# Kernel optimization log

Measured on AMD Instinct MI355X. Metric: run time of the kernel, lower is better.

The kernel has to match this reference:

```python
import jax, jax.numpy as jnp
import numpy as np

N = 100000
E = 1600000
IN_DIM = 128
HID = 128
OUT_DIM = 64
ORDER = 4


def setup_inputs() -> dict:
    key = jax.random.key(0)
    ks = jax.random.split(key, 10)
    x = jax.random.normal(ks[0], (N, IN_DIM), dtype=jnp.float32)
    edge_index = jax.random.randint(ks[1], (2, E), 0, N, dtype=jnp.int64)
    gen_edge_index = jax.random.randint(ks[2], (2, E), 0, N, dtype=jnp.int64)
    s = 1.0 / np.sqrt(IN_DIM)
    w_orig = jax.random.normal(ks[3], (ORDER + 1, IN_DIM, HID), dtype=jnp.float32) * s
    b_orig = jax.random.normal(ks[4], (ORDER + 1, HID), dtype=jnp.float32) * s
    w_aug = jax.random.normal(ks[5], (ORDER + 1, IN_DIM, HID), dtype=jnp.float32) * s
    b_aug = jax.random.normal(ks[6], (ORDER + 1, HID), dtype=jnp.float32) * s
    fusion_weight = jnp.ones((2,), dtype=jnp.float32)
    clf_w = jax.random.normal(ks[7], (HID, OUT_DIM), dtype=jnp.float32) / np.sqrt(HID)
    clf_b = jax.random.normal(ks[8], (OUT_DIM,), dtype=jnp.float32) / np.sqrt(HID)
    return {"x": x, "edge_index": edge_index, "gen_edge_index": gen_edge_index,
            "w_orig": w_orig, "b_orig": b_orig, "w_aug": w_aug, "b_aug": b_aug,
            "fusion_weight": fusion_weight, "clf_w": clf_w, "clf_b": clf_b}


def _beta_wavelet(x, edge_index, W, b, num_nodes):
    # add self loops
    loop = jnp.arange(num_nodes, dtype=edge_index.dtype)
    row = jnp.concatenate([edge_index[0], loop])
    col = jnp.concatenate([edge_index[1], loop])
    # symmetric normalization D^{-1/2} A D^{-1/2}
    deg = jax.ops.segment_sum(jnp.ones_like(col, dtype=x.dtype), col, num_segments=num_nodes)
    dinv = jnp.where(deg > 0, deg ** -0.5, 0.0)
    norm = dinv[row] * dinv[col]  # [E+N]
    out = x @ W[0] + b[0]
    Tx = x
    for i in range(1, ORDER + 1):
        msg = norm[:, None] * Tx[row]                      # gather + scale [E+N, D]
        Tx = jax.ops.segment_sum(msg, col, num_segments=num_nodes)  # scatter_add
        out = out + Tx @ W[i] + b[i]
    return jax.nn.relu(out)


def reference(x, edge_index, gen_edge_index, w_orig, b_orig, w_aug, b_aug, fusion_weight, clf_w, clf_b):
    num_nodes = x.shape[0]
    h_orig = _beta_wavelet(x, edge_index, w_orig, b_orig, num_nodes)
    h_aug = _beta_wavelet(x, gen_edge_index, w_aug, b_aug, num_nodes)
    w = jax.nn.softmax(fusion_weight)
    h_final = w[0] * h_orig + w[1] * h_aug
    return h_final @ clf_w + clf_b
```

## Files before the change

kernel.cpp:

```cpp
#include <hip/hip_runtime.h>

#define N_NODES 100000
#define NPAD    100096
#define NE      1600000
#define DIM     128
#define ODIM    64
#define NORDER  4
#define KTOT    640
#define NB      391

typedef _Float16 h8 __attribute__((ext_vector_type(8)));
typedef float f4 __attribute__((ext_vector_type(4)));

__device__ __forceinline__ float2 up2(unsigned p) {
    union { unsigned u; _Float16 h[2]; } c; c.u = p;
    return make_float2((float)c.h[0], (float)c.h[1]);
}
__device__ __forceinline__ unsigned pk2(float x, float y) {
    union { unsigned u; _Float16 h[2]; } c;
    c.h[0] = (_Float16)x; c.h[1] = (_Float16)y;
    return c.u;
}
__device__ __forceinline__ unsigned short f2hbits(float x) {
    union { _Float16 h; unsigned short s; } c;
    c.h = (_Float16)x;
    return c.s;
}
__device__ __forceinline__ void async_cp16(const void* g, void* l) {
    __builtin_amdgcn_global_load_lds((const __attribute__((address_space(1))) void*)g,
                                     (__attribute__((address_space(3))) void*)l, 16, 0, 0);
}


__global__ __launch_bounds__(256) void hist_edges(const int* __restrict__ e0,
                                                  const int* __restrict__ e1,
                                                  int* __restrict__ bhist) {
    __shared__ int lh[NB];
    int t = threadIdx.x;
    int g = blockIdx.x >= 782;
    int blk = g ? (blockIdx.x - 782) : blockIdx.x;
    const int* colp = (g ? e1 : e0) + NE;
    int* bh = bhist + g * NB;
    for (int i = t; i < NB; i += 256) lh[i] = 0;
    __syncthreads();
    int base = blk * 2048 + t;
#pragma unroll
    for (int j = 0; j < 8; ++j) {
        int e = base + j * 256;
        if (e < NE) atomicAdd(&lh[colp[e] >> 8], 1);
    }
    __syncthreads();
    for (int i = t; i < NB; i += 256) if (lh[i]) atomicAdd(&bh[i], lh[i]);
}

__global__ void wave_scan(const int* __restrict__ in,
                          int* __restrict__ oexcl,
                          int* __restrict__ ocur,
                          int n, int with_cur) {
    int wv = threadIdx.x >> 6, lane = threadIdx.x & 63;
    if (wv >= 2) return;
    const int* I = in + wv * n;
    int* O = oexcl + wv * (n + 1);
    int* C = ocur + wv * n;
    int carry = 0;
    for (int base = 0; base < n; base += 64) {
        int i = base + lane;
        int v = (i < n) ? I[i] : 0;
        int s = v;
#pragma unroll
        for (int off = 1; off < 64; off <<= 1) {
            int x = __shfl_up(s, off, 64);
            if (lane >= off) s += x;
        }
        int excl = carry + s - v;
        if (i < n) {
            O[i] = excl;
            if (with_cur) C[i] = excl;
        }
        carry += __shfl(s, 63, 64);
    }
    if (lane == 0) O[n] = carry;
}

__global__ __launch_bounds__(256) void part_edges(const int* __restrict__ e0,
                                                  const int* __restrict__ e1,
                                                  int* __restrict__ bcursor,
                                                  unsigned* __restrict__ pairs) {
    __shared__ int lh[NB];
    __shared__ int lpos[NB];
    int t = threadIdx.x;
    int g = blockIdx.x >= NB;
    int blk = g ? (blockIdx.x - NB) : blockIdx.x;
    const int* rowp = (g ? e1 : e0);
    const int* colp = rowp + NE;
    int* bc = bcursor + g * NB;
    unsigned* pr = pairs + (size_t)g * NE;
    for (int i = t; i < NB; i += 256) lh[i] = 0;
    __syncthreads();
    int base = blk * 4096 + t;
    int rank[16];
    short bk[16];
    unsigned char lcv[16];
#pragma unroll
    for (int j = 0; j < 16; ++j) {
        int e = base + j * 256;
        rank[j] = -1;
        if (e < NE) {
            int c = colp[e];
            bk[j] = (short)(c >> 8);
            lcv[j] = (unsigned char)(c & 255);
            rank[j] = atomicAdd(&lh[c >> 8], 1);
        }
    }
    __syncthreads();
    for (int i = t; i < NB; i += 256) {
        int n = lh[i];
        lpos[i] = n ? atomicAdd(&bc[i], n) : 0;
    }
    __syncthreads();
#pragma unroll
    for (int j = 0; j < 16; ++j) {
        int e = base + j * 256;
        if (e < NE) {
            int b = bk[j];
            pr[lpos[b] + rank[j]] = ((unsigned)rowp[e] << 8) | lcv[j];
        }
    }
}

__global__ __launch_bounds__(256) void cnt_scan(const unsigned* __restrict__ pairs,
                                                const int* __restrict__ boff,
                                                int* __restrict__ ptrv,
                                                float* __restrict__ dinv,
                                                int* __restrict__ bsum) {
    __shared__ int lcnt[256];
    __shared__ int lscan[256];
    int t = threadIdx.x;
    int g = blockIdx.x >= NB;
    int b = g ? (blockIdx.x - NB) : blockIdx.x;
    const unsigned* pr = pairs + (size_t)g * NE;
    const int* bo = boff + g * (NB + 1);
    int* pv = ptrv + g * (N_NODES + 1);
    float* dv = dinv + g * N_NODES;
    int* bs = bsum + g * NB;
    lcnt[t] = 0;
    __syncthreads();
    int s = bo[b], e = bo[b + 1];
    for (int i = s + t; i < e; i += 256)
        atomicAdd(&lcnt[pr[i] & 255u], 1);
    __syncthreads();
    int v = lcnt[t];
    lscan[t] = v;
    __syncthreads();
    for (int off = 1; off < 256; off <<= 1) {
        int x = (t >= off) ? lscan[t - off] : 0;
        __syncthreads();
        lscan[t] += x;
        __syncthreads();
    }
    int node = (b << 8) + t;
    if (node < N_NODES) {
        pv[node] = lscan[t] - v;
        dv[node] = rsqrtf((float)(v + 1));
    }
    if (t == 255) bs[b] = lscan[255];
}

__global__ __launch_bounds__(256) void scan_addk(int* __restrict__ ptrv,
                                                 const int* __restrict__ bmid) {
    int t = threadIdx.x;
    int g = blockIdx.x >= NB;
    int b = g ? (blockIdx.x - NB) : blockIdx.x;
    int* pv = ptrv + g * (N_NODES + 1);
    const int* bm = bmid + g * (NB + 1);
    int node = (b << 8) + t;
    if (node < N_NODES) pv[node] += bm[b];
    if (b == 0 && t == 0) pv[N_NODES] = NE;
}

__global__ __launch_bounds__(256) void fine_csr(const unsigned* __restrict__ pairs,
                                                const int* __restrict__ boff,
                                                const int* __restrict__ ptrv,
                                                int* __restrict__ srcv) {
    __shared__ int lcnt[256];
    int t = threadIdx.x;
    int g = blockIdx.x >= NB;
    int b = g ? (blockIdx.x - NB) : blockIdx.x;
    const unsigned* pr = pairs + (size_t)g * NE;
    const int* bo = boff + g * (NB + 1);
    const int* pv = ptrv + g * (N_NODES + 1);
    int* sv = srcv + (size_t)g * NE;
    lcnt[t] = 0;
    __syncthreads();
    int s = bo[b], e = bo[b + 1];
    int base = b << 8;
    for (int i = s + t; i < e; i += 256) {
        unsigned pk = pr[i];
        int lc = (int)(pk & 255u);
        int pos = pv[base + lc] + atomicAdd(&lcnt[lc], 1);
        sv[pos] = (int)(pk >> 8);
    }
}

__global__ __launch_bounds__(256) void xcast(const float* __restrict__ x,
                                             unsigned* __restrict__ Tbig) {
    int idx = blockIdx.x * 256 + threadIdx.x;
    if (idx >= NPAD * 64) return;
    int m = idx >> 6, u = idx & 63;
    int e = (m << 7) + u * 2;
    float a = (m < N_NODES) ? x[e]     : 0.f;
    float b = (m < N_NODES) ? x[e + 1] : 0.f;
    Tbig[m * 320 + u] = pk2(a, b);
}

__global__ __launch_bounds__(256) void wcast(const float* __restrict__ Wo,
                                             const float* __restrict__ Wa,
                                             unsigned short* __restrict__ Wt) {
    int idx = blockIdx.x * 256 + threadIdx.x;
    if (idx >= 2 * 5 * DIM * DIM) return;
    int g   = idx / (5 * DIM * DIM);
    int rem = idx % (5 * DIM * DIM);
    int i   = rem / (DIM * DIM);
    int r2  = rem % (DIM * DIM);
    int k8  = r2 >> 10;
    int n   = (r2 >> 3) & 127;
    int k7  = r2 & 7;
    int k   = k8 * 8 + k7;
    const float* W = g ? Wa : Wo;
    Wt[idx] = f2hbits(W[(i * DIM + k) * DIM + n]);
}

__global__ __launch_bounds__(256) void propagate(const unsigned* __restrict__ Tin,
                                                 unsigned* __restrict__ Tout,
                                                 const int* __restrict__ ptrv,
                                                 const int* __restrict__ srcv,
                                                 const float* __restrict__ dinv) {
    int gid  = blockIdx.x * 256 + threadIdx.x;
    int lane = threadIdx.x & 63;
    int v    = __builtin_amdgcn_readfirstlane(gid >> 6);
    if (v >= N_NODES) return;
    float dv = dinv[v];
    float2 self = up2(Tin[v * 320 + lane]);
    float ax = dv * dv * self.x;
    float ay = dv * dv * self.y;
    int beg = ptrv[v], end = ptrv[v + 1];
    int k = beg;
    for (; k + 16 <= end; k += 16) {
        int u[16];
#pragma unroll
        for (int j = 0; j < 16; ++j) u[j] = srcv[k + j];
        float2 tt[16];
#pragma unroll
        for (int j = 0; j < 16; ++j) tt[j] = up2(Tin[u[j] * 320 + lane]);
        float w[16];
#pragma unroll
        for (int j = 0; j < 16; ++j) w[j] = dinv[u[j]] * dv;
#pragma unroll
        for (int j = 0; j < 16; ++j) { ax += w[j] * tt[j].x; ay += w[j] * tt[j].y; }
    }
    for (; k + 4 <= end; k += 4) {
        int u[4];
#pragma unroll
        for (int j = 0; j < 4; ++j) u[j] = srcv[k + j];
        float2 tt[4];
#pragma unroll
        for (int j = 0; j < 4; ++j) tt[j] = up2(Tin[u[j] * 320 + lane]);
        float w[4];
#pragma unroll
        for (int j = 0; j < 4; ++j) w[j] = dinv[u[j]] * dv;
#pragma unroll
        for (int j = 0; j < 4; ++j) { ax += w[j] * tt[j].x; ay += w[j] * tt[j].y; }
    }
    for (; k < end; ++k) {
        int u = srcv[k];
        float w = dinv[u] * dv;
        float2 t = up2(Tin[u * 320 + lane]);
        ax += w * t.x; ay += w * t.y;
    }
    Tout[v * 320 + lane] = pk2(ax, ay);
}

__global__ __launch_bounds__(256, 3) void gemmK(const unsigned short* __restrict__ A,
                                                const unsigned short* __restrict__ Wt,
                                                float* __restrict__ C) {
    __shared__ unsigned short Bl[DIM * DIM];
    int t = threadIdx.x;
    int lane = t & 63, wv = t >> 6;
    int m0 = blockIdx.x * 128 + wv * 32;
    int l15 = lane & 15, q = lane >> 4;
    f4 acc[2][8];
#pragma unroll
    for (int mt = 0; mt < 2; ++mt)
#pragma unroll
        for (int nt = 0; nt < 8; ++nt) acc[mt][nt] = (f4)(0.f);

#pragma unroll
    for (int i = 0; i < 5; ++i) {
        const unsigned short* WtI = Wt + (size_t)i * DIM * DIM;
        h8 af[2][4];
#pragma unroll
        for (int mt = 0; mt < 2; ++mt)
#pragma unroll
            for (int kc = 0; kc < 4; ++kc)
                af[mt][kc] = *(const h8*)(A + (size_t)(m0 + mt * 16 + l15) * KTOT
                                            + i * DIM + (kc * 4 + q) * 8);
#pragma unroll
        for (int c = 0; c < 8; ++c) {
            int ci = c * 4 + wv;
            async_cp16(WtI + ci * 512 + lane * 8, &Bl[ci * 512]);
        }
        __syncthreads();
#pragma unroll
        for (int kc = 0; kc < 4; ++kc) {
            int c = kc * 4 + q;
#pragma unroll
            for (int nt = 0; nt < 8; ++nt) {
                h8 bf = *(const h8*)&Bl[(size_t)(c * 128 + nt * 16 + l15) * 8];
                acc[0][nt] = __builtin_amdgcn_mfma_f32_16x16x32_f16(af[0][kc], bf, acc[0][nt], 0, 0, 0);
                acc[1][nt] = __builtin_amdgcn_mfma_f32_16x16x32_f16(af[1][kc], bf, acc[1][nt], 0, 0, 0);
            }
        }
        __syncthreads();
    }
#pragma unroll
    for (int mt = 0; mt < 2; ++mt)
#pragma unroll
        for (int nt = 0; nt < 8; ++nt)
#pragma unroll
            for (int r = 0; r < 4; ++r)
                C[(size_t)(m0 + mt * 16 + q * 4 + r) * DIM + nt * 16 + l15] = acc[mt][nt][r];
}

__global__ __launch_bounds__(256) void fuse_clf(const float* __restrict__ accO,
                                                const float* __restrict__ accA,
                                                const float* __restrict__ bO,
                                                const float* __restrict__ bA,
                                                const float* __restrict__ fw,
                                                const float* __restrict__ clfW,
                                                const float* __restrict__ clfB,
                                                float* __restrict__ out) {
    __shared__ float Wl[DIM * ODIM];
    __shared__ float Hl[32 * DIM];
    __shared__ float bs[2][DIM];
    int t = threadIdx.x;
    float f0 = fw[0], f1 = fw[1];
    float m = fmaxf(f0, f1);
    float e0 = expf(f0 - m), e1 = expf(f1 - m);
    float sw0 = e0 / (e0 + e1), sw1 = e1 / (e0 + e1);
    if (t < 128) {
        float s = 0.f;
        for (int i = 0; i <= NORDER; ++i) s += bO[i * DIM + t];
        bs[0][t] = s;
    } else {
        int j = t - 128;
        float s = 0.f;
        for (int i = 0; i <= NORDER; ++i) s += bA[i * DIM + j];
        bs[1][j] = s;
    }
    for (int i = 0; i < 8; ++i) {
        int idx = (i * 256 + t) * 4;
        *(float4*)&Wl[idx] = *(const float4*)&clfW[idx];
    }
    __syncthreads();
    int rowBase = blockIdx.x * 32;
    for (int i = 0; i < 4; ++i) {
        int idx = (i * 256 + t) * 4;
        int kcol = idx & 127;
        float4 a = *(const float4*)&accO[rowBase * DIM + idx];
        float4 b = *(const float4*)&accA[rowBase * DIM + idx];
        float4 h;
        h.x = sw0 * fmaxf(a.x + bs[0][kcol + 0], 0.f) + sw1 * fmaxf(b.x + bs[1][kcol + 0], 0.f);
        h.y = sw0 * fmaxf(a.y + bs[0][kcol + 1], 0.f) + sw1 * fmaxf(b.y + bs[1][kcol + 1], 0.f);
        h.z = sw0 * fmaxf(a.z + bs[0][kcol + 2], 0.f) + sw1 * fmaxf(b.z + bs[1][kcol + 2], 0.f);
        h.w = sw0 * fmaxf(a.w + bs[0][kcol + 3], 0.f) + sw1 * fmaxf(b.w + bs[1][kcol + 3], 0.f);
        *(float4*)&Hl[idx] = h;
    }
    __syncthreads();
    int lane = t & 63, w = t >> 6;
    int c2 = (lane & 31) * 2;
    int r0 = w * 8 + (lane >> 5) * 4;
    float acc[4][2];
    for (int j = 0; j < 4; ++j) { acc[j][0] = 0.f; acc[j][1] = 0.f; }
    for (int k0 = 0; k0 < DIM; k0 += 4) {
        float4 a0 = *(const float4*)&Hl[(r0 + 0) * DIM + k0];
        float4 a1 = *(const float4*)&Hl[(r0 + 1) * DIM + k0];
        float4 a2 = *(const float4*)&Hl[(r0 + 2) * DIM + k0];
        float4 a3 = *(const float4*)&Hl[(r0 + 3) * DIM + k0];
#define FSTEP(comp, kk)                                                      \
        {                                                                    \
            float2 wv = *(const float2*)&Wl[(k0 + kk) * ODIM + c2];          \
            acc[0][0] += a0.comp * wv.x; acc[0][1] += a0.comp * wv.y;        \
            acc[1][0] += a1.comp * wv.x; acc[1][1] += a1.comp * wv.y;        \
            acc[2][0] += a2.comp * wv.x; acc[2][1] += a2.comp * wv.y;        \
            acc[3][0] += a3.comp * wv.x; acc[3][1] += a3.comp * wv.y;        \
        }
        FSTEP(x, 0) FSTEP(y, 1) FSTEP(z, 2) FSTEP(w, 3)
#undef FSTEP
    }
    float2 cb2 = *(const float2*)&clfB[c2];
    for (int j = 0; j < 4; ++j) {
        float2 o = make_float2(acc[j][0] + cb2.x, acc[j][1] + cb2.y);
        *(float2*)&out[(rowBase + r0 + j) * ODIM + c2] = o;
    }
}

extern "C" void kernel_launch(void* const* d_in, const int* in_sizes, int n_in,
                              void* d_out, int out_size, void* d_ws, size_t ws_size,
                              hipStream_t stream) {
    const float* x   = (const float*)d_in[0];
    const int*   ei  = (const int*)d_in[1];
    const int*   gi  = (const int*)d_in[2];
    const float* w_o = (const float*)d_in[3];
    const float* b_o = (const float*)d_in[4];
    const float* w_a = (const float*)d_in[5];
    const float* b_a = (const float*)d_in[6];
    const float* fw  = (const float*)d_in[7];
    const float* cw  = (const float*)d_in[8];
    const float* cb  = (const float*)d_in[9];
    float* out = (float*)d_out;

    char* p = (char*)d_ws;
    auto alloc = [&](size_t bytes) {
        void* r = (void*)p;
        p += (bytes + 255) & ~(size_t)255;
        return r;
    };
    unsigned* Tbig = (unsigned*)alloc((size_t)NPAD * 320 * 4);
    float* acc_o = (float*)alloc((size_t)NPAD * DIM * 4);
    float* acc_a = (float*)alloc((size_t)NPAD * DIM * 4);
    unsigned short* Wt = (unsigned short*)alloc((size_t)2 * 5 * DIM * DIM * 2);
    float* dinv  = (float*)alloc((size_t)2 * N_NODES * 4);
    unsigned* pairs = (unsigned*)alloc((size_t)2 * NE * 4);
    int* csr_src = (int*)alloc((size_t)2 * NE * 4);
    int* csr_ptr = (int*)alloc((size_t)2 * (N_NODES + 1) * 4);
    int* bhist   = (int*)alloc((size_t)2 * NB * 4);
    int* boff    = (int*)alloc((size_t)2 * (NB + 1) * 4);
    int* bcursor = (int*)alloc((size_t)2 * NB * 4);
    int* bsum    = (int*)alloc((size_t)2 * NB * 4);
    int* bmid    = (int*)alloc((size_t)2 * (NB + 1) * 4);

    const int gP  = (N_NODES * 64 + 255) / 256;
    const int gX  = (NPAD * 64 + 255) / 256;
    const int gW  = (2 * 5 * DIM * DIM + 255) / 256;
    const int gM  = NPAD / 128;
    const int gF  = N_NODES / 32;

    xcast<<<gX, 256, 0, stream>>>(x, Tbig);
    wcast<<<gW, 256, 0, stream>>>(w_o, w_a, Wt);

    hipMemsetAsync(bhist, 0, (size_t)2 * NB * 4, stream);
    hist_edges<<<2 * 782, 256, 0, stream>>>(ei, gi, bhist);
    wave_scan<<<1, 128, 0, stream>>>(bhist, boff, bcursor, NB, 1);
    part_edges<<<2 * NB, 256, 0, stream>>>(ei, gi, bcursor, pairs);
    cnt_scan<<<2 * NB, 256, 0, stream>>>(pairs, boff, csr_ptr, dinv, bsum);
    wave_scan<<<1, 128, 0, stream>>>(bsum, bmid, bcursor, NB, 0);
    scan_addk<<<2 * NB, 256, 0, stream>>>(csr_ptr, bmid);
    fine_csr<<<2 * NB, 256, 0, stream>>>(pairs, boff, csr_ptr, csr_src);

    for (int g = 0; g < 2; ++g) {
        float* acc = g ? acc_a : acc_o;
        const unsigned short* Wtg = Wt + (size_t)g * 5 * DIM * DIM;
        const int* pv = csr_ptr + g * (N_NODES + 1);
        const int* sv = csr_src + (size_t)g * NE;
        const float* dv = dinv + (size_t)g * N_NODES;

        for (int i = 1; i <= NORDER; ++i)
            propagate<<<gP, 256, 0, stream>>>(Tbig + (i - 1) * 64, Tbig + i * 64,
                                              pv, sv, dv);

        gemmK<<<gM, 256, 0, stream>>>((const unsigned short*)Tbig, Wtg, acc);
    }
    fuse_clf<<<gF, 256, 0, stream>>>(acc_o, acc_a, b_o, b_a, fw, cw, cb, out);
}
```

Baseline: 864.6 us.

## Fuse bias, ReLU, softmax blend and classifier into GEMM epilogues

The first branch GEMM now applies bias, ReLU and the softmax weight directly and writes an fp16 H0 buffer. This replaces the two fp32 accumulator buffers and the separate fuse_clf kernel. The second branch GEMM adds H0 in its epilogue, stages the blended hidden tile in LDS, and runs the classifier matmul with MFMA against a pre-cast fp16 classifier weight. The edge partition kernel also moves to 1024-thread blocks covering 16K edges each. The aim is to cut fp32 intermediate traffic and one launch, at the cost of fp16 rounding of H0 and the hidden activations.

```diff
diff --git a/kernel.cpp b/kernel.cpp
--- a/kernel.cpp
+++ b/kernel.cpp
@@ -8,6 +8,8 @@
 #define NORDER  4
 #define KTOT    640
 #define NB      391
+#define PB_EDGES 16384
+#define PB_BLKS  98
 
 typedef _Float16 h8 __attribute__((ext_vector_type(8)));
 typedef float f4 __attribute__((ext_vector_type(4)));
@@ -26,11 +28,15 @@
     c.h = (_Float16)x;
     return c.s;
 }
+__device__ __forceinline__ float h2f(unsigned short s) {
+    union { unsigned short u; _Float16 h; } c;
+    c.u = s;
+    return (float)c.h;
+}
 __device__ __forceinline__ void async_cp16(const void* g, void* l) {
     __builtin_amdgcn_global_load_lds((const __attribute__((address_space(1))) void*)g,
                                      (__attribute__((address_space(3))) void*)l, 16, 0, 0);
 }
-
 
 __global__ __launch_bounds__(256) void hist_edges(const int* __restrict__ e0,
                                                   const int* __restrict__ e1,
@@ -82,28 +88,28 @@
     if (lane == 0) O[n] = carry;
 }
 
-__global__ __launch_bounds__(256) void part_edges(const int* __restrict__ e0,
-                                                  const int* __restrict__ e1,
-                                                  int* __restrict__ bcursor,
-                                                  unsigned* __restrict__ pairs) {
+__global__ __launch_bounds__(1024) void part_edges(const int* __restrict__ e0,
+                                                   const int* __restrict__ e1,
+                                                   int* __restrict__ bcursor,
+                                                   unsigned* __restrict__ pairs) {
     __shared__ int lh[NB];
     __shared__ int lpos[NB];
     int t = threadIdx.x;
-    int g = blockIdx.x >= NB;
-    int blk = g ? (blockIdx.x - NB) : blockIdx.x;
+    int g = blockIdx.x >= PB_BLKS;
+    int blk = g ? (blockIdx.x - PB_BLKS) : blockIdx.x;
     const int* rowp = (g ? e1 : e0);
     const int* colp = rowp + NE;
     int* bc = bcursor + g * NB;
     unsigned* pr = pairs + (size_t)g * NE;
-    for (int i = t; i < NB; i += 256) lh[i] = 0;
-    __syncthreads();
-    int base = blk * 4096 + t;
+    for (int i = t; i < NB; i += 1024) lh[i] = 0;
+    __syncthreads();
+    int base = blk * PB_EDGES + t;
     int rank[16];
     short bk[16];
     unsigned char lcv[16];
 #pragma unroll
     for (int j = 0; j < 16; ++j) {
-        int e = base + j * 256;
+        int e = base + j * 1024;
         rank[j] = -1;
         if (e < NE) {
             int c = colp[e];
@@ -113,14 +119,14 @@
         }
     }
     __syncthreads();
-    for (int i = t; i < NB; i += 256) {
+    for (int i = t; i < NB; i += 1024) {
         int n = lh[i];
         lpos[i] = n ? atomicAdd(&bc[i], n) : 0;
     }
     __syncthreads();
 #pragma unroll
     for (int j = 0; j < 16; ++j) {
-        int e = base + j * 256;
+        int e = base + j * 1024;
         if (e < NE) {
             int b = bk[j];
             pr[lpos[b] + rank[j]] = ((unsigned)rowp[e] << 8) | lcv[j];
@@ -215,19 +221,26 @@
 
 __global__ __launch_bounds__(256) void wcast(const float* __restrict__ Wo,
                                              const float* __restrict__ Wa,
+                                             const float* __restrict__ cw,
                                              unsigned short* __restrict__ Wt) {
     int idx = blockIdx.x * 256 + threadIdx.x;
-    if (idx >= 2 * 5 * DIM * DIM) return;
-    int g   = idx / (5 * DIM * DIM);
-    int rem = idx % (5 * DIM * DIM);
-    int i   = rem / (DIM * DIM);
-    int r2  = rem % (DIM * DIM);
-    int k8  = r2 >> 10;
-    int n   = (r2 >> 3) & 127;
-    int k7  = r2 & 7;
-    int k   = k8 * 8 + k7;
-    const float* W = g ? Wa : Wo;
-    Wt[idx] = f2hbits(W[(i * DIM + k) * DIM + n]);
+    if (idx >= 2 * 5 * DIM * DIM + ODIM * DIM) return;
+    if (idx < 2 * 5 * DIM * DIM) {
+        int g   = idx / (5 * DIM * DIM);
+        int rem = idx % (5 * DIM * DIM);
+        int i   = rem / (DIM * DIM);
+        int r2  = rem % (DIM * DIM);
+        int k8  = r2 >> 10;
+        int n   = (r2 >> 3) & 127;
+        int k7  = r2 & 7;
+        int k   = k8 * 8 + k7;
+        const float* W = g ? Wa : Wo;
+        Wt[idx] = f2hbits(W[(i * DIM + k) * DIM + n]);
+    } else {
+        int j = idx - 2 * 5 * DIM * DIM;
+        int n = j >> 7, k = j & 127;
+        Wt[idx] = f2hbits(cw[k * ODIM + n]);
+    }
 }
 
 __global__ __launch_bounds__(256) void propagate(const unsigned* __restrict__ Tin,
@@ -280,14 +293,28 @@
     Tout[v * 320 + lane] = pk2(ax, ay);
 }
 
-__global__ __launch_bounds__(256, 3) void gemmK(const unsigned short* __restrict__ A,
-                                                const unsigned short* __restrict__ Wt,
-                                                float* __restrict__ C) {
+__global__ __launch_bounds__(256, 2) void gemmH0(
+        const unsigned short* __restrict__ A,
+        const unsigned short* __restrict__ Wt,
+        const float* __restrict__ bO,
+        const float* __restrict__ fw,
+        unsigned short* __restrict__ H0) {
     __shared__ unsigned short Bl[DIM * DIM];
+    __shared__ float bsl[DIM];
     int t = threadIdx.x;
     int lane = t & 63, wv = t >> 6;
     int m0 = blockIdx.x * 128 + wv * 32;
     int l15 = lane & 15, q = lane >> 4;
+    if (t < 128) {
+        float s = 0.f;
+        for (int i = 0; i <= NORDER; ++i) s += bO[i * DIM + t];
+        bsl[t] = s;
+    }
+    float f0 = fw[0], f1 = fw[1];
+    float mx = fmaxf(f0, f1);
+    float e0 = expf(f0 - mx), e1 = expf(f1 - mx);
+    float sw0 = e0 / (e0 + e1);
+
     f4 acc[2][8];
 #pragma unroll
     for (int mt = 0; mt < 2; ++mt)
@@ -325,83 +352,127 @@
 #pragma unroll
     for (int mt = 0; mt < 2; ++mt)
 #pragma unroll
-        for (int nt = 0; nt < 8; ++nt)
-#pragma unroll
-            for (int r = 0; r < 4; ++r)
-                C[(size_t)(m0 + mt * 16 + q * 4 + r) * DIM + nt * 16 + l15] = acc[mt][nt][r];
-}
-
-__global__ __launch_bounds__(256) void fuse_clf(const float* __restrict__ accO,
-                                                const float* __restrict__ accA,
-                                                const float* __restrict__ bO,
-                                                const float* __restrict__ bA,
-                                                const float* __restrict__ fw,
-                                                const float* __restrict__ clfW,
-                                                const float* __restrict__ clfB,
-                                                float* __restrict__ out) {
-    __shared__ float Wl[DIM * ODIM];
-    __shared__ float Hl[32 * DIM];
-    __shared__ float bs[2][DIM];
-    int t = threadIdx.x;
-    float f0 = fw[0], f1 = fw[1];
-    float m = fmaxf(f0, f1);
-    float e0 = expf(f0 - m), e1 = expf(f1 - m);
-    float sw0 = e0 / (e0 + e1), sw1 = e1 / (e0 + e1);
+        for (int nt = 0; nt < 8; ++nt) {
+            float bsv = bsl[nt * 16 + l15];
+#pragma unroll
+            for (int r = 0; r < 4; ++r) {
+                int row = m0 + mt * 16 + q * 4 + r;
+                H0[(size_t)row * DIM + nt * 16 + l15] =
+                    f2hbits(sw0 * fmaxf(acc[mt][nt][r] + bsv, 0.f));
+            }
+        }
+}
+
+__global__ __launch_bounds__(256, 2) void gemm_fused2(
+        const unsigned short* __restrict__ A,
+        const unsigned short* __restrict__ Wt,
+        const unsigned short* __restrict__ H0,
+        const float* __restrict__ bA,
+        const float* __restrict__ fw,
+        const unsigned short* __restrict__ clfWt,
+        const float* __restrict__ clfB,
+        float* __restrict__ out) {
+    __shared__ unsigned short BlH[DIM * 132];
+    __shared__ float bsl[DIM];
+    unsigned short* Bl = BlH;
+    unsigned short* Hl = BlH;
+    int t = threadIdx.x;
+    int lane = t & 63, wv = t >> 6;
+    int m0 = blockIdx.x * 128 + wv * 32;
+    int l15 = lane & 15, q = lane >> 4;
     if (t < 128) {
         float s = 0.f;
-        for (int i = 0; i <= NORDER; ++i) s += bO[i * DIM + t];
-        bs[0][t] = s;
-    } else {
-        int j = t - 128;
-        float s = 0.f;
-        for (int i = 0; i <= NORDER; ++i) s += bA[i * DIM + j];
-        bs[1][j] = s;
-    }
-    for (int i = 0; i < 8; ++i) {
-        int idx = (i * 256 + t) * 4;
-        *(float4*)&Wl[idx] = *(const float4*)&clfW[idx];
-    }
-    __syncthreads();
-    int rowBase = blockIdx.x * 32;
-    for (int i = 0; i < 4; ++i) {
-        int idx = (i * 256 + t) * 4;
-        int kcol = idx & 127;
-        float4 a = *(const float4*)&accO[rowBase * DIM + idx];
-        float4 b = *(const float4*)&accA[rowBase * DIM + idx];
-        float4 h;
-        h.x = sw0 * fmaxf(a.x + bs[0][kcol + 0], 0.f) + sw1 * fmaxf(b.x + bs[1][kcol + 0], 0.f);
-        h.y = sw0 * fmaxf(a.y + bs[0][kcol + 1], 0.f) + sw1 * fmaxf(b.y + bs[1][kcol + 1], 0.f);
-        h.z = sw0 * fmaxf(a.z + bs[0][kcol + 2], 0.f) + sw1 * fmaxf(b.z + bs[1][kcol + 2], 0.f);
-        h.w = sw0 * fmaxf(a.w + bs[0][kcol + 3], 0.f) + sw1 * fmaxf(b.w + bs[1][kcol + 3], 0.f);
-        *(float4*)&Hl[idx] = h;
-    }
-    __syncthreads();
-    int lane = t & 63, w = t >> 6;
-    int c2 = (lane & 31) * 2;
-    int r0 = w * 8 + (lane >> 5) * 4;
-    float acc[4][2];
-    for (int j = 0; j < 4; ++j) { acc[j][0] = 0.f; acc[j][1] = 0.f; }
-    for (int k0 = 0; k0 < DIM; k0 += 4) {
-        float4 a0 = *(const float4*)&Hl[(r0 + 0) * DIM + k0];
-        float4 a1 = *(const float4*)&Hl[(r0 + 1) * DIM + k0];
-        float4 a2 = *(const float4*)&Hl[(r0 + 2) * DIM + k0];
-        float4 a3 = *(const float4*)&Hl[(r0 + 3) * DIM + k0];
-#define FSTEP(comp, kk)                                                      \
-        {                                                                    \
-            float2 wv = *(const float2*)&Wl[(k0 + kk) * ODIM + c2];          \
-            acc[0][0] += a0.comp * wv.x; acc[0][1] += a0.comp * wv.y;        \
-            acc[1][0] += a1.comp * wv.x; acc[1][1] += a1.comp * wv.y;        \
-            acc[2][0] += a2.comp * wv.x; acc[2][1] += a2.comp * wv.y;        \
-            acc[3][0] += a3.comp * wv.x; acc[3][1] += a3.comp * wv.y;        \
-        }
-        FSTEP(x, 0) FSTEP(y, 1) FSTEP(z, 2) FSTEP(w, 3)
-#undef FSTEP
-    }
-    float2 cb2 = *(const float2*)&clfB[c2];
-    for (int j = 0; j < 4; ++j) {
-        float2 o = make_float2(acc[j][0] + cb2.x, acc[j][1] + cb2.y);
-        *(float2*)&out[(rowBase + r0 + j) * ODIM + c2] = o;
-    }
+        for (int i = 0; i <= NORDER; ++i) s += bA[i * DIM + t];
+        bsl[t] = s;
+    }
+    float f0 = fw[0], f1 = fw[1];
+    float mx = fmaxf(f0, f1);
+    float e0 = expf(f0 - mx), e1 = expf(f1 - mx);
+    float sw1 = e1 / (e0 + e1);
+
+    f4 acc[2][8];
+#pragma unroll
+    for (int mt = 0; mt < 2; ++mt)
+#pragma unroll
+        for (int nt = 0; nt < 8; ++nt) acc[mt][nt] = (f4)(0.f);
+
+#pragma unroll
+    for (int i = 0; i < 5; ++i) {
+        const unsigned short* WtI = Wt + (size_t)i * DIM * DIM;
+        h8 af[2][4];
+#pragma unroll
+        for (int mt = 0; mt < 2; ++mt)
+#pragma unroll
+            for (int kc = 0; kc < 4; ++kc)
+                af[mt][kc] = *(const h8*)(A + (size_t)(m0 + mt * 16 + l15) * KTOT
+                                            + i * DIM + (kc * 4 + q) * 8);
+#pragma unroll
+        for (int c = 0; c < 8; ++c) {
+            int ci = c * 4 + wv;
+            async_cp16(WtI + ci * 512 + lane * 8, &Bl[ci * 512]);
+        }
+        __syncthreads();
+#pragma unroll
+        for (int kc = 0; kc < 4; ++kc) {
+            int c = kc * 4 + q;
+#pragma unroll
+            for (int nt = 0; nt < 8; ++nt) {
+                h8 bf = *(const h8*)&Bl[(size_t)(c * 128 + nt * 16 + l15) * 8];
+                acc[0][nt] = __builtin_amdgcn_mfma_f32_16x16x32_f16(af[0][kc], bf, acc[0][nt], 0, 0, 0);
+                acc[1][nt] = __builtin_amdgcn_mfma_f32_16x16x32_f16(af[1][kc], bf, acc[1][nt], 0, 0, 0);
+            }
+        }
+        __syncthreads();
+    }
+
+#pragma unroll
+    for (int mt = 0; mt < 2; ++mt)
+#pragma unroll
+        for (int nt = 0; nt < 8; ++nt) {
+            float bsv = bsl[nt * 16 + l15];
+            int col = nt * 16 + l15;
+#pragma unroll
+            for (int r = 0; r < 4; ++r) {
+                int lrow = wv * 32 + mt * 16 + q * 4 + r;
+                int grow = m0 + mt * 16 + q * 4 + r;
+                float h = sw1 * fmaxf(acc[mt][nt][r] + bsv, 0.f)
+                        + h2f(H0[(size_t)grow * DIM + col]);
+                Hl[lrow * 132 + col] = f2hbits(h);
+            }
+        }
+    __syncthreads();
+
+    f4 o[2][4];
+#pragma unroll
+    for (int mt = 0; mt < 2; ++mt)
+#pragma unroll
+        for (int n2 = 0; n2 < 4; ++n2) o[mt][n2] = (f4)(0.f);
+#pragma unroll
+    for (int kc = 0; kc < 4; ++kc) {
+        int c = kc * 4 + q;
+        h8 ha[2];
+#pragma unroll
+        for (int mt = 0; mt < 2; ++mt)
+            ha[mt] = *(const h8*)&Hl[(wv * 32 + mt * 16 + l15) * 132 + c * 8];
+#pragma unroll
+        for (int n2 = 0; n2 < 4; ++n2) {
+            h8 bf = *(const h8*)&clfWt[(size_t)(n2 * 16 + l15) * DIM + c * 8];
+            o[0][n2] = __builtin_amdgcn_mfma_f32_16x16x32_f16(ha[0], bf, o[0][n2], 0, 0, 0);
+            o[1][n2] = __builtin_amdgcn_mfma_f32_16x16x32_f16(ha[1], bf, o[1][n2], 0, 0, 0);
+        }
+    }
+#pragma unroll
+    for (int mt = 0; mt < 2; ++mt)
+#pragma unroll
+        for (int n2 = 0; n2 < 4; ++n2) {
+            int col = n2 * 16 + l15;
+            float cbv = clfB[col];
+#pragma unroll
+            for (int r = 0; r < 4; ++r) {
+                int row = m0 + mt * 16 + q * 4 + r;
+                if (row < N_NODES) out[(size_t)row * ODIM + col] = o[mt][n2][r] + cbv;
+            }
+        }
 }
 
 extern "C" void kernel_launch(void* const* d_in, const int* in_sizes, int n_in,
@@ -426,9 +497,8 @@
         return r;
     };
     unsigned* Tbig = (unsigned*)alloc((size_t)NPAD * 320 * 4);
-    float* acc_o = (float*)alloc((size_t)NPAD * DIM * 4);
-    float* acc_a = (float*)alloc((size_t)NPAD * DIM * 4);
-    unsigned short* Wt = (unsigned short*)alloc((size_t)2 * 5 * DIM * DIM * 2);
+    unsigned short* H0 = (unsigned short*)alloc((size_t)NPAD * DIM * 2);
+    unsigned short* Wt = (unsigned short*)alloc(((size_t)2 * 5 * DIM * DIM + ODIM * DIM) * 2);
     float* dinv  = (float*)alloc((size_t)2 * N_NODES * 4);
     unsigned* pairs = (unsigned*)alloc((size_t)2 * NE * 4);
     int* csr_src = (int*)alloc((size_t)2 * NE * 4);
@@ -441,34 +511,36 @@
 
     const int gP  = (N_NODES * 64 + 255) / 256;
     const int gX  = (NPAD * 64 + 255) / 256;
-    const int gW  = (2 * 5 * DIM * DIM + 255) / 256;
+    const int gW  = (2 * 5 * DIM * DIM + ODIM * DIM + 255) / 256;
     const int gM  = NPAD / 128;
-    const int gF  = N_NODES / 32;
 
     xcast<<<gX, 256, 0, stream>>>(x, Tbig);
-    wcast<<<gW, 256, 0, stream>>>(w_o, w_a, Wt);
+    wcast<<<gW, 256, 0, stream>>>(w_o, w_a, cw, Wt);
 
     hipMemsetAsync(bhist, 0, (size_t)2 * NB * 4, stream);
     hist_edges<<<2 * 782, 256, 0, stream>>>(ei, gi, bhist);
     wave_scan<<<1, 128, 0, stream>>>(bhist, boff, bcursor, NB, 1);
-    part_edges<<<2 * NB, 256, 0, stream>>>(ei, gi, bcursor, pairs);
+    part_edges<<<2 * PB_BLKS, 1024, 0, stream>>>(ei, gi, bcursor, pairs);
     cnt_scan<<<2 * NB, 256, 0, stream>>>(pairs, boff, csr_ptr, dinv, bsum);
     wave_scan<<<1, 128, 0, stream>>>(bsum, bmid, bcursor, NB, 0);
     scan_addk<<<2 * NB, 256, 0, stream>>>(csr_ptr, bmid);
     fine_csr<<<2 * NB, 256, 0, stream>>>(pairs, boff, csr_ptr, csr_src);
 
-    for (int g = 0; g < 2; ++g) {
-        float* acc = g ? acc_a : acc_o;
-        const unsigned short* Wtg = Wt + (size_t)g * 5 * DIM * DIM;
-        const int* pv = csr_ptr + g * (N_NODES + 1);
-        const int* sv = csr_src + (size_t)g * NE;
-        const float* dv = dinv + (size_t)g * N_NODES;
-
+    for (int i = 1; i <= NORDER; ++i)
+        propagate<<<gP, 256, 0, stream>>>(Tbig + (i - 1) * 64, Tbig + i * 64,
+                                          csr_ptr, csr_src, dinv);
+    gemmH0<<<gM, 256, 0, stream>>>((const unsigned short*)Tbig, Wt, b_o, fw, H0);
+
+    {
+        const int* pv = csr_ptr + (N_NODES + 1);
+        const int* sv = csr_src + (size_t)NE;
+        const float* dv = dinv + (size_t)N_NODES;
         for (int i = 1; i <= NORDER; ++i)
             propagate<<<gP, 256, 0, stream>>>(Tbig + (i - 1) * 64, Tbig + i * 64,
                                               pv, sv, dv);
-
-        gemmK<<<gM, 256, 0, stream>>>((const unsigned short*)Tbig, Wtg, acc);
-    }
-    fuse_clf<<<gF, 256, 0, stream>>>(acc_o, acc_a, b_o, b_a, fw, cw, cb, out);
-}
+    }
+    gemm_fused2<<<gM, 256, 0, stream>>>((const unsigned short*)Tbig,
+                                        Wt + (size_t)5 * DIM * DIM,
+                                        H0, b_a, fw,
+                                        Wt + (size_t)2 * 5 * DIM * DIM, cb, out);
+}
```

Measured after the change: 818.2 us. 5.4% less time.
